# Optimization experiments

Hardware: AMD Instinct MI355X
Metric: run time of the kernel (lower is better)

Reference implementation:

```python
import jax, jax.numpy as jnp
import numpy as np

B, N, DIN, DOUT = 8192, 4, 1024, 256

def setup_inputs() -> dict:
    key = jax.random.key(0)
    k1, k2, k3, k4 = jax.random.split(key, 4)
    adj = jax.random.uniform(k1, (N, N), dtype=jnp.float32)
    features = jax.random.normal(k2, (B, N, DIN), dtype=jnp.float32)
    # nn.Linear(input_size, output_size): weight [DOUT, DIN], bias [DOUT]
    bound = 1.0 / np.sqrt(DIN)
    W = jax.random.uniform(k3, (DOUT, DIN), dtype=jnp.float32, minval=-bound, maxval=bound)
    b = jax.random.uniform(k4, (DOUT,), dtype=jnp.float32, minval=-bound, maxval=bound)
    return {"adj": adj, "features": features, "W": W, "b": b}

def reference(adj, features, W, b):
    # Batched equivalent of: for i in B: linear(adj @ features[i]) -> [B, 4, DOUT]
    h = jnp.einsum("nm,bmf->bnf", adj, features)  # [B, N, DIN]
    return jnp.einsum("bnf,of->bno", h, W) + b    # [B, N, DOUT]
```

## Files before the change

kernel.cpp:

```cpp
#include <hip/hip_runtime.h>


#define DIN 1024
#define DOUT 256
#define BM 32
#define KI 16
#define LDB 72
#define A_HALFS (BM * LDB)

typedef __bf16 bf16x8 __attribute__((ext_vector_type(8)));
typedef float f32x4 __attribute__((ext_vector_type(4)));
typedef unsigned short u16x8 __attribute__((ext_vector_type(8)));

__device__ __forceinline__ unsigned short f2bf(float f) {
  union { float f; unsigned int u; } v;
  v.f = f;
  unsigned int u = v.u;
  u += 0x7fffu + ((u >> 16) & 1u);
  return (unsigned short)(u >> 16);
}

__device__ __forceinline__ u16x8 pack8(f32x4 lo, f32x4 hi) {
  u16x8 r;
#pragma unroll
  for (int m = 0; m < 4; ++m) {
    r[m] = f2bf(lo[m]);
    r[4 + m] = f2bf(hi[m]);
  }
  return r;
}

__global__ __launch_bounds__(256) void wprep_kernel(
    const float* __restrict__ W, unsigned short* __restrict__ ws) {
  const int t = blockIdx.x * 256 + threadIdx.x;
  const int lane = t & 63;
  const int j = (t >> 6) & 3;
  const int ks = (t >> 8) & 1;
  const int kb = (t >> 9) & 15;
  const int g = (t >> 13) & 3;
  const int col = g * 64 + j * 16 + (lane & 15);
  const int k0 = kb * 64 + ks * 32 + (lane >> 4) * 8;
  const f32x4* src = (const f32x4*)(W + (size_t)col * DIN + k0);
  f32x4 a = src[0], b = src[1];
  *(u16x8*)(ws + (size_t)t * 8) = pack8(a, b);
}

__global__ __launch_bounds__(256, 3) void gconv_kernel(
    const float* __restrict__ adj, const float* __restrict__ feat,
    const unsigned short* __restrict__ wbf, const float* __restrict__ bias,
    float* __restrict__ out) {
  __shared__ __align__(16) unsigned short sA[4][2][A_HALFS];

  const int tid = threadIdx.x;
  const int bM = blockIdx.x * BM;

  const int lane = tid & 63;
  const int wid = tid >> 6;
  const int wc = wid * 64;
  const int rl = lane & 15;
  const int q = lane >> 4;
  const int q8 = q * 8;

  const int arow = lane >> 3;
  const int ac8 = (lane & 7) * 8;
  const float* abase = feat + (size_t)(bM + arow) * DIN + ac8;
  unsigned short* swl = &sA[wid][0][arow * LDB + ac8];

  const unsigned short* bp = wbf + (size_t)wid * 128 * 512 + lane * 8;

  f32x4 acc[2][4];
#pragma unroll
  for (int i = 0; i < 2; ++i)
#pragma unroll
    for (int j = 0; j < 4; ++j) acc[i][j] = f32x4{0.f, 0.f, 0.f, 0.f};

  f32x4 pf[4][2];
#pragma unroll
  for (int v = 0; v < 4; ++v) {
    pf[v][0] = *(const f32x4*)(abase + (size_t)v * 8 * DIN);
    pf[v][1] = *(const f32x4*)(abase + (size_t)v * 8 * DIN + 4);
  }
#pragma unroll
  for (int v = 0; v < 4; ++v)
    *(u16x8*)(swl + v * 8 * LDB) = pack8(pf[v][0], pf[v][1]);
#pragma unroll
  for (int v = 0; v < 4; ++v) {
    pf[v][0] = *(const f32x4*)(abase + (size_t)v * 8 * DIN + 64);
    pf[v][1] = *(const f32x4*)(abase + (size_t)v * 8 * DIN + 68);
  }

  for (int kb = 0; kb < KI; ++kb) {
    bf16x8 bfr[2][4];
#pragma unroll
    for (int ks = 0; ks < 2; ++ks)
#pragma unroll
      for (int j = 0; j < 4; ++j)
        bfr[ks][j] = *(const bf16x8*)(bp + ((kb * 2 + ks) * 4 + j) * 512);

    const unsigned short* sa = &sA[wid][kb & 1][0];
    bf16x8 af[2][2];
#pragma unroll
    for (int i = 0; i < 2; ++i)
#pragma unroll
      for (int ks = 0; ks < 2; ++ks)
        af[i][ks] = *(const bf16x8*)(sa + (i * 16 + rl) * LDB + ks * 32 + q8);

#pragma unroll
    for (int ks = 0; ks < 2; ++ks)
#pragma unroll
      for (int i = 0; i < 2; ++i)
#pragma unroll
        for (int j = 0; j < 4; ++j)
          acc[i][j] = __builtin_amdgcn_mfma_f32_16x16x32_bf16(
              af[i][ks], bfr[ks][j], acc[i][j], 0, 0, 0);

    if (kb + 1 < KI) {
      unsigned short* sw = swl + ((kb + 1) & 1) * A_HALFS;
#pragma unroll
      for (int v = 0; v < 4; ++v)
        *(u16x8*)(sw + v * 8 * LDB) = pack8(pf[v][0], pf[v][1]);
      if (kb + 2 < KI) {
#pragma unroll
        for (int v = 0; v < 4; ++v) {
          pf[v][0] =
              *(const f32x4*)(abase + (size_t)v * 8 * DIN + (kb + 2) * 64);
          pf[v][1] =
              *(const f32x4*)(abase + (size_t)v * 8 * DIN + (kb + 2) * 64 + 4);
        }
      }
    }
  }

  float am[16];
#pragma unroll
  for (int i = 0; i < 16; ++i) am[i] = adj[i];

  float bv[4];
#pragma unroll
  for (int j = 0; j < 4; ++j) bv[j] = bias[wc + j * 16 + rl];

#pragma unroll
  for (int i = 0; i < 2; ++i) {
    const size_t rowbase = (size_t)(bM + i * 16 + q * 4);
#pragma unroll
    for (int j = 0; j < 4; ++j) {
      const int col = wc + j * 16 + rl;
      float* op = out + rowbase * DOUT + col;
      f32x4 g = acc[i][j];
#pragma unroll
      for (int n = 0; n < 4; ++n) {
        op[(size_t)n * DOUT] = am[n * 4 + 0] * g[0] + am[n * 4 + 1] * g[1] +
                               am[n * 4 + 2] * g[2] + am[n * 4 + 3] * g[3] +
                               bv[j];
      }
    }
  }
}

extern "C" void kernel_launch(void* const* d_in, const int* in_sizes, int n_in,
                              void* d_out, int out_size, void* d_ws,
                              size_t ws_size, hipStream_t stream) {
  const float* adj = (const float*)d_in[0];
  const float* feat = (const float*)d_in[1];
  const float* W = (const float*)d_in[2];
  const float* bias = (const float*)d_in[3];
  float* out = (float*)d_out;
  unsigned short* ws = (unsigned short*)d_ws;

  wprep_kernel<<<128, 256, 0, stream>>>(W, ws);
  gconv_kernel<<<8192 * 4 / BM, 256, 0, stream>>>(adj, feat, ws, bias, out);
}
```

Baseline: 231.4 us.

## Pre-pack features into bf16 MFMA fragment layout in a separate prep kernel

Adds an fprep kernel that converts the fp32 features to bf16 and writes them into a workspace image already arranged in the MFMA A-fragment order. The main GEMM kernel then loads A fragments directly from global memory, dropping its LDS staging buffers, register prefetch and in-loop packing. The aim is a shorter, simpler inner loop with no LDS traffic. The cost is an extra full pass over the feature tensor (read fp32, write bf16, read bf16 again), and each of the four waves in a block now fetches the same A data from global memory or cache.

```diff
diff --git a/kernel.cpp b/kernel.cpp
--- a/kernel.cpp
+++ b/kernel.cpp
@@ -5,8 +5,6 @@
 #define DOUT 256
 #define BM 32
 #define KI 16
-#define LDB 72
-#define A_HALFS (BM * LDB)
 
 typedef __bf16 bf16x8 __attribute__((ext_vector_type(8)));
 typedef float f32x4 __attribute__((ext_vector_type(4)));
@@ -45,12 +43,28 @@
   *(u16x8*)(ws + (size_t)t * 8) = pack8(a, b);
 }
 
+__global__ __launch_bounds__(256) void fprep_kernel(
+    const float* __restrict__ feat, unsigned short* __restrict__ fs) {
+  const int t = blockIdx.x * 256 + threadIdx.x;
+  const int k8 = t & 127;
+  const int row = t >> 7;
+  const f32x4* src = (const f32x4*)(feat + (size_t)row * DIN + k8 * 8);
+  f32x4 a = src[0], b = src[1];
+  const int m = row >> 5;
+  const int i = (row >> 4) & 1;
+  const int rl = row & 15;
+  const int kb = k8 >> 3;
+  const int ks = (k8 >> 2) & 1;
+  const int q = k8 & 3;
+  const size_t off =
+      (((size_t)m * 64 + (i * 16 + kb) * 2 + ks) * 512) + (q * 16 + rl) * 8;
+  *(u16x8*)(fs + off) = pack8(a, b);
+}
+
 __global__ __launch_bounds__(256, 3) void gconv_kernel(
-    const float* __restrict__ adj, const float* __restrict__ feat,
-    const unsigned short* __restrict__ wbf, const float* __restrict__ bias,
+    const float* __restrict__ adj, const unsigned short* __restrict__ fimg,
+    const unsigned short* __restrict__ wimg, const float* __restrict__ bias,
     float* __restrict__ out) {
-  __shared__ __align__(16) unsigned short sA[4][2][A_HALFS];
-
   const int tid = threadIdx.x;
   const int bM = blockIdx.x * BM;
 
@@ -59,14 +73,9 @@
   const int wc = wid * 64;
   const int rl = lane & 15;
   const int q = lane >> 4;
-  const int q8 = q * 8;
 
-  const int arow = lane >> 3;
-  const int ac8 = (lane & 7) * 8;
-  const float* abase = feat + (size_t)(bM + arow) * DIN + ac8;
-  unsigned short* swl = &sA[wid][0][arow * LDB + ac8];
-
-  const unsigned short* bp = wbf + (size_t)wid * 128 * 512 + lane * 8;
+  const unsigned short* ap = fimg + (size_t)blockIdx.x * 64 * 512 + lane * 8;
+  const unsigned short* bp = wimg + (size_t)wid * 128 * 512 + lane * 8;
 
   f32x4 acc[2][4];
 #pragma unroll
@@ -74,36 +83,21 @@
 #pragma unroll
     for (int j = 0; j < 4; ++j) acc[i][j] = f32x4{0.f, 0.f, 0.f, 0.f};
 
-  f32x4 pf[4][2];
 #pragma unroll
-  for (int v = 0; v < 4; ++v) {
-    pf[v][0] = *(const f32x4*)(abase + (size_t)v * 8 * DIN);
-    pf[v][1] = *(const f32x4*)(abase + (size_t)v * 8 * DIN + 4);
-  }
+  for (int kb = 0; kb < KI; ++kb) {
+    bf16x8 af[2][2];
 #pragma unroll
-  for (int v = 0; v < 4; ++v)
-    *(u16x8*)(swl + v * 8 * LDB) = pack8(pf[v][0], pf[v][1]);
+    for (int i = 0; i < 2; ++i)
 #pragma unroll
-  for (int v = 0; v < 4; ++v) {
-    pf[v][0] = *(const f32x4*)(abase + (size_t)v * 8 * DIN + 64);
-    pf[v][1] = *(const f32x4*)(abase + (size_t)v * 8 * DIN + 68);
-  }
+      for (int ks = 0; ks < 2; ++ks)
+        af[i][ks] = *(const bf16x8*)(ap + ((i * 16 + kb) * 2 + ks) * 512);
 
-  for (int kb = 0; kb < KI; ++kb) {
     bf16x8 bfr[2][4];
 #pragma unroll
     for (int ks = 0; ks < 2; ++ks)
 #pragma unroll
       for (int j = 0; j < 4; ++j)
         bfr[ks][j] = *(const bf16x8*)(bp + ((kb * 2 + ks) * 4 + j) * 512);
-
-    const unsigned short* sa = &sA[wid][kb & 1][0];
-    bf16x8 af[2][2];
-#pragma unroll
-    for (int i = 0; i < 2; ++i)
-#pragma unroll
-      for (int ks = 0; ks < 2; ++ks)
-        af[i][ks] = *(const bf16x8*)(sa + (i * 16 + rl) * LDB + ks * 32 + q8);
 
 #pragma unroll
     for (int ks = 0; ks < 2; ++ks)
@@ -113,22 +107,6 @@
         for (int j = 0; j < 4; ++j)
           acc[i][j] = __builtin_amdgcn_mfma_f32_16x16x32_bf16(
               af[i][ks], bfr[ks][j], acc[i][j], 0, 0, 0);
-
-    if (kb + 1 < KI) {
-      unsigned short* sw = swl + ((kb + 1) & 1) * A_HALFS;
-#pragma unroll
-      for (int v = 0; v < 4; ++v)
-        *(u16x8*)(sw + v * 8 * LDB) = pack8(pf[v][0], pf[v][1]);
-      if (kb + 2 < KI) {
-#pragma unroll
-        for (int v = 0; v < 4; ++v) {
-          pf[v][0] =
-              *(const f32x4*)(abase + (size_t)v * 8 * DIN + (kb + 2) * 64);
-          pf[v][1] =
-              *(const f32x4*)(abase + (size_t)v * 8 * DIN + (kb + 2) * 64 + 4);
-        }
-      }
-    }
   }
 
   float am[16];
@@ -166,7 +144,10 @@
   const float* bias = (const float*)d_in[3];
   float* out = (float*)d_out;
   unsigned short* ws = (unsigned short*)d_ws;
+  unsigned short* wimg = ws;
+  unsigned short* fimg = ws + 262144;
 
-  wprep_kernel<<<128, 256, 0, stream>>>(W, ws);
-  gconv_kernel<<<8192 * 4 / BM, 256, 0, stream>>>(adj, feat, ws, bias, out);
+  wprep_kernel<<<128, 256, 0, stream>>>(W, wimg);
+  fprep_kernel<<<16384, 256, 0, stream>>>(feat, fimg);
+  gconv_kernel<<<8192 * 4 / BM, 256, 0, stream>>>(adj, fimg, wimg, bias, out);
 }
```

After: 292.1 us. +26.2%, slower.
